# Optimization experiments

Hardware: AMD Instinct MI355X
Metric: run time of the kernel (lower is better)

Reference implementation:

```python
import jax, jax.numpy as jnp
import numpy as np

N = 50000      # nodes
E = 800000     # edges (avg degree 16)
F_IN = 512     # num_feature
H = 256        # nhid


def setup_inputs() -> dict:
    key = jax.random.key(0)
    ks = jax.random.split(key, 40)
    def p(k, shape):
        return jax.random.normal(k, shape, jnp.float32) * 0.05
    inp = {}
    inp["x"] = jax.random.normal(ks[0], (N, F_IN), jnp.float32)
    src = jax.random.randint(ks[1], (E,), 0, N, jnp.int32)
    dst = jax.random.randint(ks[2], (E,), 0, N, jnp.int32)
    inp["edge_index"] = jnp.stack([src, dst])  # [2, E]
    # GIN conv MLPs: Lin(din,H), ReLU, Lin(H,H). Weights stored [in, out].
    dims = [F_IN, H, H, H]
    i = 3
    for li, din in enumerate(dims, 1):
        inp[f"c{li}w1"] = p(ks[i], (din, H)); i += 1
        inp[f"c{li}b1"] = p(ks[i], (H,)); i += 1
        inp[f"c{li}w2"] = p(ks[i], (H, H)); i += 1
        inp[f"c{li}b2"] = p(ks[i], (H,)); i += 1
    # 2-layer LSTM, gate order i,f,g,o; single fused bias (b_ih + b_hh).
    for l in range(2):
        inp[f"lstm{l}_wih"] = p(ks[i], (H, 4 * H)); i += 1
        inp[f"lstm{l}_whh"] = p(ks[i], (H, 4 * H)); i += 1
        inp[f"lstm{l}_b"] = p(ks[i], (4 * H,)); i += 1
    inp["mlp_w"] = p(ks[i], (H, H)); i += 1
    inp["mlp_b"] = p(ks[i], (H,))
    return inp


def _gin(h, src, dst, w1, b1, w2, b2):
    # GINConv with eps=0: nn(x + sum_{j->i} x_j)
    agg = jax.ops.segment_sum(h[src], dst, num_segments=N)
    z = jax.nn.relu((h + agg) @ w1 + b1)
    return z @ w2 + b2


def _lstm_layer(seq, wih, whh, b):
    # seq: [T, N, H] -> hidden states [T, N, H]
    def step(carry, xt):
        h, c = carry
        g = xt @ wih + h @ whh + b
        i, f, gg, o = jnp.split(g, 4, axis=-1)
        c = jax.nn.sigmoid(f) * c + jax.nn.sigmoid(i) * jnp.tanh(gg)
        h = jax.nn.sigmoid(o) * jnp.tanh(c)
        return (h, c), h
    h0 = jnp.zeros((seq.shape[1], whh.shape[0]), seq.dtype)
    _, hs = jax.lax.scan(step, (h0, h0), seq)
    return hs


def reference(x, edge_index, c1w1, c1b1, c1w2, c1b2, c2w1, c2b1, c2w2, c2b2,
              c3w1, c3b1, c3w2, c3b2, c4w1, c4b1, c4w2, c4b2,
              lstm0_wih, lstm0_whh, lstm0_b, lstm1_wih, lstm1_whh, lstm1_b,
              mlp_w, mlp_b):
    src, dst = edge_index[0], edge_index[1]
    x1 = jax.nn.relu(_gin(x, src, dst, c1w1, c1b1, c1w2, c1b2))
    x2 = jax.nn.relu(_gin(x1, src, dst, c2w1, c2b1, c2w2, c2b2))
    x3 = jax.nn.relu(_gin(x2, src, dst, c3w1, c3b1, c3w2, c3b2))
    x4 = jax.nn.relu(_gin(x3, src, dst, c4w1, c4b1, c4w2, c4b2))
    # residual sums (in-place cascade as in the original)
    x2 = x2 + x1
    x3 = x3 + x2
    x4 = x4 + x3
    x_sum = x1 + x2 + x3 + x4
    stack = jnp.stack([x_sum, x1, x2, x3, x4])  # [5, N, H]
    x_avg = stack.mean(axis=0)
    x_max = stack.max(axis=0)
    seq = jnp.stack([x1, x2, x3, x4])  # [4, N, H]
    h = _lstm_layer(seq, lstm0_wih, lstm0_whh, lstm0_b)
    h = _lstm_layer(h, lstm1_wih, lstm1_whh, lstm1_b)
    x_lstm = h.mean(axis=0)
    # channel attention: relu(mlp(x_avg) + mlp(x_max) + mlp(x_lstm))
    return jax.nn.relu((x_avg + x_max + x_lstm) @ mlp_w + 3.0 * mlp_b)
```

## Files before the change

kernel.cpp:

```cpp
#include <hip/hip_runtime.h>

typedef unsigned int u32;
typedef unsigned short u16;

typedef __attribute__((ext_vector_type(8))) __bf16 bf16x8;
typedef __attribute__((ext_vector_type(4))) float f32x4;

__device__ __forceinline__ u16 f2bf(float f) {
  u32 u = __float_as_uint(f);
  u += 0x7fffu + ((u >> 16) & 1u);
  return (u16)(u >> 16);
}
__device__ __forceinline__ float bl(u32 u) { return __uint_as_float(u << 16); }
__device__ __forceinline__ float bh(u32 u) { return __uint_as_float(u & 0xffff0000u); }
__device__ __forceinline__ u32 pk2(float a, float b) { return (u32)f2bf(a) | ((u32)f2bf(b) << 16); }
__device__ __forceinline__ float fsig(float x) { return 1.f / (1.f + __expf(-x)); }
__device__ __forceinline__ float ftanh(float x) { return 1.f - 2.f / (__expf(2.f * x) + 1.f); }

#define GLDS16(gp, lp)                                                                  \
  __builtin_amdgcn_global_load_lds((const __attribute__((address_space(1))) u32*)(gp),  \
                                   (__attribute__((address_space(3))) u32*)(lp), 16, 0, 0)

struct WTargs {
  const float* src[13];
  u16* dst[13];
  int K[13];
  int Nc[13];
  int bstart[14];
};
__global__ __launch_bounds__(256) void k_wtall(WTargs wa) {
  int b = blockIdx.x;
  int w = 0;
  while (b >= wa.bstart[w + 1]) ++w;
  int i = (b - wa.bstart[w]) * 256 + threadIdx.x;
  int K = wa.K[w], Nc = wa.Nc[w];
  if (i >= K * Nc) return;
  int k = i / Nc, c = i - k * Nc;
  wa.dst[w][(size_t)c * K + k] = f2bf(wa.src[w][i]);
}

__global__ __launch_bounds__(256) void k_x2bf(const float* __restrict__ x, u16* __restrict__ xb, int total8) {
  int i = blockIdx.x * 256 + threadIdx.x;
  if (i >= total8) return;
  size_t o = (size_t)i * 8;
  float4 a = *(const float4*)(x + o), b = *(const float4*)(x + o + 4);
  uint4 v;
  v.x = pk2(a.x, a.y); v.y = pk2(a.z, a.w); v.z = pk2(b.x, b.y); v.w = pk2(b.z, b.w);
  *(uint4*)(xb + o) = v;
}

__global__ void k_hist(const int* __restrict__ dst, int* __restrict__ deg, int E) {
  int e = blockIdx.x * 256 + threadIdx.x;
  if (e < E) atomicAdd(&deg[dst[e]], 1);
}
__global__ __launch_bounds__(1024) void k_scan1(const int* __restrict__ deg, int* __restrict__ rs,
                                                int* __restrict__ bsum, int n) {
  __shared__ int buf[1024];
  int t = threadIdx.x, idx = blockIdx.x * 1024 + t;
  int v = idx < n ? deg[idx] : 0;
  buf[t] = v;
  __syncthreads();
  for (int off = 1; off < 1024; off <<= 1) {
    int u = t >= off ? buf[t - off] : 0;
    __syncthreads();
    buf[t] += u;
    __syncthreads();
  }
  if (idx < n) rs[idx + 1] = buf[t];
  if (t == 1023) bsum[blockIdx.x] = buf[1023];
}
__global__ void k_scan2(int* bsum, int nb) {
  if (threadIdx.x == 0) {
    int s = 0;
    for (int b = 0; b < nb; ++b) { s += bsum[b]; bsum[b] = s; }
  }
}
__global__ void k_scan3(const int* __restrict__ bsum, int* __restrict__ rs,
                        int* __restrict__ cursor, int n) {
  int i = blockIdx.x * 256 + threadIdx.x;
  if (i >= n) return;
  int b = i >> 10;
  int add = b ? bsum[b - 1] : 0;
  int v = rs[i + 1] + add;
  int d = cursor[i];
  rs[i + 1] = v;
  cursor[i] = v - d;
  if (i == 0) rs[0] = 0;
}
__global__ void k_scatter(const int* __restrict__ src, const int* __restrict__ dst,
                          int* __restrict__ cursor, int* __restrict__ esrc, int E) {
  int e = blockIdx.x * 256 + threadIdx.x;
  if (e < E) {
    int p = atomicAdd(&cursor[dst[e]], 1);
    esrc[p] = src[e];
  }
}

__global__ __launch_bounds__(256) void k_aggbr(const u16* __restrict__ y, const int* __restrict__ rowstart,
                                               const int* __restrict__ esrc, const float* __restrict__ b1,
                                               u16* __restrict__ z, int Nn, int base, int rows) {
  int lane = threadIdx.x & 63, wid = threadIdx.x >> 6;
  int r = blockIdx.x * 4 + wid;
  if (r >= rows) return;
  int node = base + r;
  const int cb = lane * 4;
  u16* orow = z + (size_t)r * 256 + cb;
  if (node >= Nn) { *(uint2*)orow = uint2{0, 0}; return; }
  float acc[4];
  {
    uint2 v = *(const uint2*)(y + (size_t)node * 256 + cb);
    acc[0] = bl(v.x); acc[1] = bh(v.x); acc[2] = bl(v.y); acc[3] = bh(v.y);
  }
  int s = rowstart[node], e = rowstart[node + 1];
  int j = s;
  for (; j + 3 < e; j += 4) {
    uint2 v0 = *(const uint2*)(y + (size_t)esrc[j] * 256 + cb);
    uint2 v1 = *(const uint2*)(y + (size_t)esrc[j + 1] * 256 + cb);
    uint2 v2 = *(const uint2*)(y + (size_t)esrc[j + 2] * 256 + cb);
    uint2 v3 = *(const uint2*)(y + (size_t)esrc[j + 3] * 256 + cb);
    acc[0] += (bl(v0.x) + bl(v1.x)) + (bl(v2.x) + bl(v3.x));
    acc[1] += (bh(v0.x) + bh(v1.x)) + (bh(v2.x) + bh(v3.x));
    acc[2] += (bl(v0.y) + bl(v1.y)) + (bl(v2.y) + bl(v3.y));
    acc[3] += (bh(v0.y) + bh(v1.y)) + (bh(v2.y) + bh(v3.y));
  }
  for (; j < e; ++j) {
    uint2 v = *(const uint2*)(y + (size_t)esrc[j] * 256 + cb);
    acc[0] += bl(v.x); acc[1] += bh(v.x); acc[2] += bl(v.y); acc[3] += bh(v.y);
  }
  float4 bb = *(const float4*)(b1 + cb);
  acc[0] = fmaxf(acc[0] + bb.x, 0.f);
  acc[1] = fmaxf(acc[1] + bb.y, 0.f);
  acc[2] = fmaxf(acc[2] + bb.z, 0.f);
  acc[3] = fmaxf(acc[3] + bb.w, 0.f);
  uint2 o;
  o.x = pk2(acc[0], acc[1]); o.y = pk2(acc[2], acc[3]);
  *(uint2*)orow = o;
}

__global__ __launch_bounds__(256) void k_agg256(const u16* __restrict__ h,
                                                const int* __restrict__ rowstart,
                                                const int* __restrict__ esrc,
                                                u16* __restrict__ out, int Nn, int base, int rows) {
  int lane = threadIdx.x & 63, wid = threadIdx.x >> 6;
  int r = blockIdx.x * 4 + wid;
  if (r >= rows) return;
  int node = base + r;
  const int cb = lane * 4;
  u16* orow = out + (size_t)r * 256 + cb;
  if (node >= Nn) { *(uint2*)orow = uint2{0, 0}; return; }
  float acc[4];
  {
    uint2 v = *(const uint2*)(h + (size_t)node * 256 + cb);
    acc[0] = bl(v.x); acc[1] = bh(v.x); acc[2] = bl(v.y); acc[3] = bh(v.y);
  }
  int s = rowstart[node], e = rowstart[node + 1];
  int j = s;
  for (; j + 3 < e; j += 4) {
    uint2 v0 = *(const uint2*)(h + (size_t)esrc[j] * 256 + cb);
    uint2 v1 = *(const uint2*)(h + (size_t)esrc[j + 1] * 256 + cb);
    uint2 v2 = *(const uint2*)(h + (size_t)esrc[j + 2] * 256 + cb);
    uint2 v3 = *(const uint2*)(h + (size_t)esrc[j + 3] * 256 + cb);
    acc[0] += (bl(v0.x) + bl(v1.x)) + (bl(v2.x) + bl(v3.x));
    acc[1] += (bh(v0.x) + bh(v1.x)) + (bh(v2.x) + bh(v3.x));
    acc[2] += (bl(v0.y) + bl(v1.y)) + (bl(v2.y) + bl(v3.y));
    acc[3] += (bh(v0.y) + bh(v1.y)) + (bh(v2.y) + bh(v3.y));
  }
  for (; j < e; ++j) {
    uint2 v = *(const uint2*)(h + (size_t)esrc[j] * 256 + cb);
    acc[0] += bl(v.x); acc[1] += bh(v.x); acc[2] += bl(v.y); acc[3] += bh(v.y);
  }
  uint2 o;
  o.x = pk2(acc[0], acc[1]); o.y = pk2(acc[2], acc[3]);
  *(uint2*)orow = o;
}

template <int BN, int MODE>
__global__ __launch_bounds__(256) void k_gemm(const u16* __restrict__ A1, const u16* __restrict__ B1, int K1,
                                              const u16* __restrict__ A2, const u16* __restrict__ B2, int K2,
                                              const float* __restrict__ bias, float bscale,
                                              void* __restrict__ outp, int Nout, int Mstore, int NT,
                                              u16* __restrict__ cstp, float* __restrict__ hsump,
                                              int first, int dosum) {
  constexpr int NF = BN / 32;
  __shared__ u16 Al[128 * 64];
  __shared__ u16 Bl[BN * 64];
  const int tid = threadIdx.x;
  const int lane = tid & 63, wid = tid >> 6;
  const int wr = wid >> 1, wc = wid & 1;
  const int nwg = gridDim.x;
  const int orig = blockIdx.x;
  const int q = nwg >> 3, rr8 = nwg & 7;
  const int xcd = orig & 7;
  const int wgid = (xcd < rr8 ? xcd * (q + 1) : rr8 * (q + 1) + (xcd - rr8) * q) + (orig >> 3);
  const int mtile = wgid / NT, ntile = wgid - mtile * NT;
  const int m0 = mtile * 128;
  const int n0 = ntile * BN;
  const int h0 = ntile * 32;
  const int l15 = lane & 15, l4 = lane >> 4;
  const int srow = lane >> 3;
  const int scol = ((lane & 7) ^ (lane >> 3)) * 8;
  const int rsw = l15 & 7;
  f32x4 acc[4][NF] = {};

  for (int s = 0; s < 2; ++s) {
    const u16* A = s ? A2 : A1;
    const u16* B = s ? B2 : B1;
    const int K = s ? K2 : K1;
    if (A == nullptr) continue;
    for (int k0 = 0; k0 < K; k0 += 64) {
      __syncthreads();
#pragma unroll
      for (int p = 0; p < 4; ++p) {
        int r = m0 + p * 32 + wid * 8 + srow;
        GLDS16(A + (size_t)r * K + k0 + scol, &Al[(p * 32 + wid * 8) * 64]);
      }
#pragma unroll
      for (int p = 0; p < NF; ++p) {
        int r;
        if constexpr (MODE == 3) r = p * 256 + h0 + wid * 8 + srow;
        else r = n0 + p * 32 + wid * 8 + srow;
        GLDS16(B + (size_t)r * K + k0 + scol, &Bl[(p * 32 + wid * 8) * 64]);
      }
      __syncthreads();
#pragma unroll
      for (int ks = 0; ks < 2; ++ks) {
        const int sp = (((ks * 4 + l4) ^ rsw)) * 8;
        bf16x8 af[4], bfr[NF];
#pragma unroll
        for (int m = 0; m < 4; ++m)
          af[m] = *(const bf16x8*)&Al[(wr * 64 + m * 16 + l15) * 64 + sp];
#pragma unroll
        for (int n = 0; n < NF; ++n) {
          int trow;
          if constexpr (MODE == 3) trow = n * 32 + wc * 16 + l15;
          else trow = wc * (BN / 2) + n * 16 + l15;
          bfr[n] = *(const bf16x8*)&Bl[trow * 64 + sp];
        }
#pragma unroll
        for (int m = 0; m < 4; ++m)
#pragma unroll
          for (int n = 0; n < NF; ++n)
            acc[m][n] = __builtin_amdgcn_mfma_f32_16x16x32_bf16(af[m], bfr[n], acc[m][n], 0, 0, 0);
      }
    }
  }

  if constexpr (MODE == 3) {
    const int hcol = h0 + wc * 16 + l15;
    const float bi = bias[hcol], bf2 = bias[256 + hcol];
    const float bg = bias[512 + hcol], bo = bias[768 + hcol];
    u16* hout = (u16*)outp;
#pragma unroll
    for (int m = 0; m < 4; ++m) {
      int gr0 = m0 + wr * 64 + m * 16 + l4 * 4;
#pragma unroll
      for (int r = 0; r < 4; ++r) {
        int gr = gr0 + r;
        if (gr >= Mstore) continue;
        float gi = acc[m][0][r] + bi;
        float gf = acc[m][1][r] + bf2;
        float gg = acc[m][2][r] + bg;
        float go = acc[m][3][r] + bo;
        size_t o = (size_t)gr * 256 + hcol;
        float nc = fsig(gi) * ftanh(gg);
        if (!first) nc += fsig(gf) * bl((u32)cstp[o]);
        cstp[o] = f2bf(nc);
        nc = bl((u32)f2bf(nc));
        float h = fsig(go) * ftanh(nc);
        hout[o] = f2bf(h);
        if (dosum) {
          if (first) hsump[o] = h;
          else hsump[o] += h;
        }
      }
    }
    return;
  }

#pragma unroll
  for (int m = 0; m < 4; ++m) {
    int gr0 = m0 + wr * 64 + m * 16 + l4 * 4;
#pragma unroll
    for (int n = 0; n < NF; ++n) {
      int gc = n0 + wc * (BN / 2) + n * 16 + l15;
      float bb = bias ? bias[gc] * bscale : 0.f;
#pragma unroll
      for (int r = 0; r < 4; ++r) {
        int gr = gr0 + r;
        if (gr >= Mstore) continue;
        float v = acc[m][n][r] + bb;
        if (MODE >= 1) v = fmaxf(v, 0.f);
        if (MODE == 2) ((float*)outp)[(size_t)gr * Nout + gc] = v;
        else ((u16*)outp)[(size_t)gr * Nout + gc] = f2bf(v);
      }
    }
  }
}

__global__ __launch_bounds__(256) void k_cascade(const u16* __restrict__ x1, u16* __restrict__ x2,
                                                 u16* __restrict__ x3, u16* __restrict__ x4, int total4) {
  int i = blockIdx.x * 256 + threadIdx.x;
  if (i >= total4) return;
  size_t o = (size_t)i * 4;
  uint2 v1 = *(const uint2*)(x1 + o), v2 = *(const uint2*)(x2 + o);
  uint2 v3 = *(const uint2*)(x3 + o), v4 = *(const uint2*)(x4 + o);
  float a1[4] = {bl(v1.x), bh(v1.x), bl(v1.y), bh(v1.y)};
  float a2[4] = {bl(v2.x), bh(v2.x), bl(v2.y), bh(v2.y)};
  float a3[4] = {bl(v3.x), bh(v3.x), bl(v3.y), bh(v3.y)};
  float a4[4] = {bl(v4.x), bh(v4.x), bl(v4.y), bh(v4.y)};
  float y2[4], y3[4], y4[4];
#pragma unroll
  for (int j = 0; j < 4; ++j) {
    y2[j] = a2[j] + a1[j];
    y3[j] = a3[j] + y2[j];
    y4[j] = a4[j] + y3[j];
  }
  *(uint2*)(x2 + o) = uint2{pk2(y2[0], y2[1]), pk2(y2[2], y2[3])};
  *(uint2*)(x3 + o) = uint2{pk2(y3[0], y3[1]), pk2(y3[2], y3[3])};
  *(uint2*)(x4 + o) = uint2{pk2(y4[0], y4[1]), pk2(y4[2], y4[3])};
}

__global__ __launch_bounds__(256) void k_sfin(const u16* __restrict__ x1, const u16* __restrict__ x2,
                                              const u16* __restrict__ x3, const u16* __restrict__ x4,
                                              const float* __restrict__ hsum, u16* __restrict__ sb,
                                              int total4) {
  int i = blockIdx.x * 256 + threadIdx.x;
  if (i >= total4) return;
  size_t o = (size_t)i * 4;
  uint2 v1 = *(const uint2*)(x1 + o), v2 = *(const uint2*)(x2 + o);
  uint2 v3 = *(const uint2*)(x3 + o), v4 = *(const uint2*)(x4 + o);
  float4 hh = *(const float4*)(hsum + o);
  float r0 = 1.4f * (bl(v1.x) + bl(v2.x) + bl(v3.x) + bl(v4.x)) + 0.25f * hh.x;
  float r1 = 1.4f * (bh(v1.x) + bh(v2.x) + bh(v3.x) + bh(v4.x)) + 0.25f * hh.y;
  float r2 = 1.4f * (bl(v1.y) + bl(v2.y) + bl(v3.y) + bl(v4.y)) + 0.25f * hh.z;
  float r3 = 1.4f * (bh(v1.y) + bh(v2.y) + bh(v3.y) + bh(v4.y)) + 0.25f * hh.w;
  *(uint2*)(sb + o) = uint2{pk2(r0, r1), pk2(r2, r3)};
}

extern "C" void kernel_launch(void* const* d_in, const int* in_sizes, int n_in,
                              void* d_out, int out_size, void* d_ws, size_t ws_size,
                              hipStream_t stream) {
  (void)n_in; (void)out_size;
  const int N = in_sizes[0] / 512;
  const int E = in_sizes[1] / 2;
  const int Mpad = ((N + 127) / 128) * 128;
  auto al128 = [](int v) { return ((v + 127) / 128) * 128; };

  const float* x = (const float*)d_in[0];
  const int* ei = (const int*)d_in[1];
  const int* esrc_in = ei;
  const int* edst_in = ei + E;

  size_t off = 0;
  auto alloc = [&](size_t bytes) { size_t o = off; off += (bytes + 255) & ~(size_t)255; return o; };
  char* ws = (char*)d_ws;
  const size_t szH = (size_t)Mpad * 256 * 2;
  const size_t szXB = (size_t)Mpad * 512 * 2;
  const int widx[13] = {2, 4, 6, 8, 10, 12, 14, 16, 18, 19, 21, 22, 24};
  const int wK[13] = {512, 256, 256, 256, 256, 256, 256, 256, 256, 256, 256, 256, 256};
  const int wN[13] = {256, 256, 256, 256, 256, 256, 256, 256, 1024, 1024, 1024, 1024, 256};
  size_t wt_o[13];
  for (int i = 0; i < 13; ++i) wt_o[i] = alloc((size_t)wK[i] * wN[i] * 2);
  size_t rowstart_o = alloc((size_t)(N + 1) * 4);
  size_t cursor_o = alloc((size_t)N * 4);
  size_t bsum_o = alloc(256 * 4);
  size_t esrc_o = alloc((size_t)E * 4);
  size_t x_o[4];
  for (int t = 0; t < 4; ++t) x_o[t] = alloc(szH);
  int McC = al128((Mpad + 3) / 4);
  int McL = al128((Mpad + 7) / 8);
  {
    const int ccand[3] = {Mpad, al128((Mpad + 1) / 2), al128((Mpad + 3) / 4)};
    const int lcand[4] = {al128((Mpad + 1) / 2), 16384, 8192, al128((Mpad + 7) / 8)};
    bool done = false;
    for (int ci = 0; ci < 3 && !done; ++ci) {
      for (int li = 0; li < 4 && !done; ++li) {
        size_t cneed = szXB + szH + (size_t)ccand[ci] * 512;
        size_t lneed = (size_t)lcand[li] * 5120;
        size_t tmp = cneed > lneed ? cneed : lneed;
        if (off + tmp + (1u << 20) <= ws_size) { McC = ccand[ci]; McL = lcand[li]; done = true; }
      }
    }
  }
  const size_t hb = (size_t)McL * 256 * 2;
  const size_t fb = (size_t)McL * 256 * 4;
  size_t lstm_sz = 8 * hb + fb;
  size_t conv_sz = szXB + szH + (size_t)McC * 512;
  size_t tmp_o = alloc(lstm_sz > conv_sz ? lstm_sz : conv_sz);
  if (off > ws_size) return;

  u16* wt[13];
  for (int i = 0; i < 13; ++i) wt[i] = (u16*)(ws + wt_o[i]);
  int* rowstart = (int*)(ws + rowstart_o);
  int* cursor = (int*)(ws + cursor_o);
  int* bsum = (int*)(ws + bsum_o);
  int* esrc = (int*)(ws + esrc_o);
  u16* xl[4];
  for (int t = 0; t < 4; ++t) xl[t] = (u16*)(ws + x_o[t]);
  u16* xb = (u16*)(ws + tmp_o);
  u16* y1 = (u16*)(ws + tmp_o + szXB);
  u16* zC = (u16*)(ws + tmp_o + szXB + szH);
  u16* h0s[4];
  for (int t = 0; t < 4; ++t) h0s[t] = (u16*)(ws + tmp_o + t * hb);
  u16* h1p[2] = {(u16*)(ws + tmp_o + 4 * hb), (u16*)(ws + tmp_o + 5 * hb)};
  u16* cst = (u16*)(ws + tmp_o + 6 * hb);
  u16* sbc = (u16*)(ws + tmp_o + 7 * hb);
  float* hsum = (float*)(ws + tmp_o + 8 * hb);

  WTargs wa;
  int bacc = 0;
  for (int i = 0; i < 13; ++i) {
    wa.src[i] = (const float*)d_in[widx[i]];
    wa.dst[i] = wt[i];
    wa.K[i] = wK[i];
    wa.Nc[i] = wN[i];
    wa.bstart[i] = bacc;
    bacc += (wK[i] * wN[i] + 255) / 256;
  }
  wa.bstart[13] = bacc;
  k_wtall<<<bacc, 256, 0, stream>>>(wa);
  k_x2bf<<<(N * 64 + 255) / 256, 256, 0, stream>>>(x, xb, N * 64);
  if (Mpad > N) hipMemsetAsync(xb + (size_t)N * 512, 0, (size_t)(Mpad - N) * 512 * 2, stream);
  hipMemsetAsync(cursor, 0, (size_t)N * 4, stream);
  k_hist<<<(E + 255) / 256, 256, 0, stream>>>(edst_in, cursor, E);
  const int nb = (N + 1023) / 1024;
  k_scan1<<<nb, 1024, 0, stream>>>(cursor, rowstart, bsum, N);
  k_scan2<<<1, 64, 0, stream>>>(bsum, nb);
  k_scan3<<<(N + 255) / 256, 256, 0, stream>>>(bsum, rowstart, cursor, N);
  k_scatter<<<(E + 255) / 256, 256, 0, stream>>>(esrc_in, edst_in, cursor, esrc, E);

  auto gemm = [&](const u16* A1, const u16* B1, int K1, const u16* A2, const u16* B2, int K2,
                  const float* bias, float bscale, void* out, int Nout, int rows, int Mstore,
                  int mode) {
    dim3 b(256);
    if (mode == 0) {
      int NT = Nout / 128;
      dim3 g((rows / 128) * NT);
      k_gemm<128, 0><<<g, b, 0, stream>>>(A1, B1, K1, A2, B2, K2, bias, bscale, out, Nout, Mstore,
                                          NT, nullptr, nullptr, 0, 0);
    } else if (mode == 1) {
      int NT = Nout / 128;
      dim3 g((rows / 128) * NT);
      k_gemm<128, 1><<<g, b, 0, stream>>>(A1, B1, K1, A2, B2, K2, bias, bscale, out, Nout, Mstore,
                                          NT, nullptr, nullptr, 0, 0);
    } else {
      int NT = Nout / 64;
      dim3 g((rows / 128) * NT);
      k_gemm<64, 2><<<g, b, 0, stream>>>(A1, B1, K1, A2, B2, K2, bias, bscale, out, Nout, Mstore,
                                         NT, nullptr, nullptr, 0, 0);
    }
  };
  auto lstm_step = [&](const u16* xt, const u16* wih, const u16* hprev, const u16* whh,
                       const float* bias, u16* hout, float* hsumP, int rows, int first, int dosum) {
    dim3 g((rows / 128) * 8), b(256);
    k_gemm<128, 3><<<g, b, 0, stream>>>(xt, wih, 256, hprev, whh, 256, bias, 1.f,
                                        hout, 256, rows, 8, cst, hsumP, first, dosum);
  };

  gemm(xb, wt[0], 512, nullptr, nullptr, 0, nullptr, 0.f, y1, 256, Mpad, Mpad, 0);
  for (int base = 0; base < Mpad; base += McC) {
    int rows = Mpad - base < McC ? Mpad - base : McC;
    int ab = (rows + 3) / 4;
    k_aggbr<<<ab, 256, 0, stream>>>(y1, rowstart, esrc, (const float*)d_in[3], zC, N, base, rows);
    gemm(zC, wt[1], 256, nullptr, nullptr, 0, (const float*)d_in[5], 1.f,
         xl[0] + (size_t)base * 256, 256, rows, rows, 1);
  }
  for (int l = 1; l < 4; ++l) {
    const int cb1[4] = {3, 7, 11, 15}, cb2[4] = {5, 9, 13, 17};
    for (int base = 0; base < Mpad; base += McC) {
      int rows = Mpad - base < McC ? Mpad - base : McC;
      int ab = (rows + 3) / 4;
      k_agg256<<<ab, 256, 0, stream>>>(xl[l - 1], rowstart, esrc, zC, N, base, rows);
      gemm((u16*)zC, wt[2 * l], 256, nullptr, nullptr, 0, (const float*)d_in[cb1[l]], 1.f,
           y1, 256, rows, rows, 1);
      gemm(y1, wt[2 * l + 1], 256, nullptr, nullptr, 0, (const float*)d_in[cb2[l]], 1.f,
           xl[l] + (size_t)base * 256, 256, rows, rows, 1);
    }
  }
  k_cascade<<<(Mpad * 64 + 255) / 256, 256, 0, stream>>>(xl[0], xl[1], xl[2], xl[3], Mpad * 64);

  const float* b_l0 = (const float*)d_in[20];
  const float* b_l1 = (const float*)d_in[23];
  const float* b_mlp = (const float*)d_in[25];
  for (int base = 0; base < Mpad; base += McL) {
    int rows = Mpad - base < McL ? Mpad - base : McL;
    const size_t boff = (size_t)base * 256;
    for (int t = 0; t < 4; ++t)
      lstm_step(xl[t] + boff, wt[8], t ? h0s[t - 1] : nullptr, wt[9], b_l0,
                h0s[t], nullptr, rows, t == 0, 0);
    for (int t = 0; t < 4; ++t)
      lstm_step(h0s[t], wt[10], t ? h1p[(t + 1) & 1] : nullptr, wt[11], b_l1,
                h1p[t & 1], hsum, rows, t == 0, 1);
    k_sfin<<<(rows * 64 + 255) / 256, 256, 0, stream>>>(xl[0] + boff, xl[1] + boff, xl[2] + boff,
                                                        xl[3] + boff, hsum, sbc, rows * 64);
    int st = N - base;
    if (st > rows) st = rows;
    if (st > 0)
      gemm(sbc, wt[12], 256, nullptr, nullptr, 0, b_mlp, 3.f,
           (float*)d_out + boff, 256, rows, st, 2);
  }
}
```

Baseline: 1.547 ms.

## Double-buffer GEMM LDS tiles to overlap global loads with MFMA

The GEMM kernel now keeps two LDS buffers for the A and B tiles. It prefetches the next K-tile with global_load_lds and waits only on the older loads through explicit vmcnt waits before computing the current tile. The two K segments are merged into one tile sequence so the prefetch carries across them. This aims to hide global memory latency behind the matrix math, at the cost of twice the LDS, which may lower occupancy. It also relies on hand-written waitcnt and barrier ordering being correct.

After: 1.824 ms. +17.9%, slower.

```diff
diff --git a/kernel.cpp b/kernel.cpp
--- a/kernel.cpp
+++ b/kernel.cpp
@@ -20,6 +20,13 @@
 #define GLDS16(gp, lp)                                                                  \
   __builtin_amdgcn_global_load_lds((const __attribute__((address_space(1))) u32*)(gp),  \
                                    (__attribute__((address_space(3))) u32*)(lp), 16, 0, 0)
+
+template <int N>
+__device__ __forceinline__ void waitvm() {
+  if constexpr (N == 8) asm volatile("s_waitcnt vmcnt(8)" ::: "memory");
+  else if constexpr (N == 6) asm volatile("s_waitcnt vmcnt(6)" ::: "memory");
+  else asm volatile("s_waitcnt vmcnt(0)" ::: "memory");
+}
 
 struct WTargs {
   const float* src[13];
@@ -182,8 +189,9 @@
                                               u16* __restrict__ cstp, float* __restrict__ hsump,
                                               int first, int dosum) {
   constexpr int NF = BN / 32;
-  __shared__ u16 Al[128 * 64];
-  __shared__ u16 Bl[BN * 64];
+  constexpr int LOADS = 4 + NF;
+  __shared__ u16 Al[2][128 * 64];
+  __shared__ u16 Bl[2][BN * 64];
   const int tid = threadIdx.x;
   const int lane = tid & 63, wid = tid >> 6;
   const int wr = wid >> 1, wc = wid & 1;
@@ -202,47 +210,61 @@
   const int rsw = l15 & 7;
   f32x4 acc[4][NF] = {};
 
-  for (int s = 0; s < 2; ++s) {
-    const u16* A = s ? A2 : A1;
-    const u16* B = s ? B2 : B1;
-    const int K = s ? K2 : K1;
-    if (A == nullptr) continue;
-    for (int k0 = 0; k0 < K; k0 += 64) {
-      __syncthreads();
-#pragma unroll
-      for (int p = 0; p < 4; ++p) {
-        int r = m0 + p * 32 + wid * 8 + srow;
-        GLDS16(A + (size_t)r * K + k0 + scol, &Al[(p * 32 + wid * 8) * 64]);
+  const int nt1 = K1 / 64;
+  const int nt2 = A2 ? K2 / 64 : 0;
+  const int nt = nt1 + nt2;
+
+  auto stage = [&](int buf, int t) {
+    const u16* A; const u16* B; int K; int k0;
+    if (t < nt1) { A = A1; B = B1; K = K1; k0 = t * 64; }
+    else { A = A2; B = B2; K = K2; k0 = (t - nt1) * 64; }
+#pragma unroll
+    for (int p = 0; p < 4; ++p) {
+      int r = m0 + p * 32 + wid * 8 + srow;
+      GLDS16(A + (size_t)r * K + k0 + scol, &Al[buf][(p * 32 + wid * 8) * 64]);
+    }
+#pragma unroll
+    for (int p = 0; p < NF; ++p) {
+      int r;
+      if constexpr (MODE == 3) r = p * 256 + h0 + wid * 8 + srow;
+      else r = n0 + p * 32 + wid * 8 + srow;
+      GLDS16(B + (size_t)r * K + k0 + scol, &Bl[buf][(p * 32 + wid * 8) * 64]);
+    }
+  };
+
+  stage(0, 0);
+  int cur = 0;
+  for (int t = 0; t < nt; ++t) {
+    if (t + 1 < nt) {
+      stage(cur ^ 1, t + 1);
+      waitvm<LOADS>();
+    } else {
+      waitvm<0>();
+    }
+    __builtin_amdgcn_s_barrier();
+#pragma unroll
+    for (int ks = 0; ks < 2; ++ks) {
+      const int sp = (((ks * 4 + l4) ^ rsw)) * 8;
+      bf16x8 af[4], bfr[NF];
+#pragma unroll
+      for (int m = 0; m < 4; ++m)
+        af[m] = *(const bf16x8*)&Al[cur][(wr * 64 + m * 16 + l15) * 64 + sp];
+#pragma unroll
+      for (int n = 0; n < NF; ++n) {
+        int trow;
+        if constexpr (MODE == 3) trow = n * 32 + wc * 16 + l15;
+        else trow = wc * (BN / 2) + n * 16 + l15;
+        bfr[n] = *(const bf16x8*)&Bl[cur][trow * 64 + sp];
       }
 #pragma unroll
-      for (int p = 0; p < NF; ++p) {
-        int r;
-        if constexpr (MODE == 3) r = p * 256 + h0 + wid * 8 + srow;
-        else r = n0 + p * 32 + wid * 8 + srow;
-        GLDS16(B + (size_t)r * K + k0 + scol, &Bl[(p * 32 + wid * 8) * 64]);
-      }
-      __syncthreads();
-#pragma unroll
-      for (int ks = 0; ks < 2; ++ks) {
-        const int sp = (((ks * 4 + l4) ^ rsw)) * 8;
-        bf16x8 af[4], bfr[NF];
-#pragma unroll
-        for (int m = 0; m < 4; ++m)
-          af[m] = *(const bf16x8*)&Al[(wr * 64 + m * 16 + l15) * 64 + sp];
-#pragma unroll
-        for (int n = 0; n < NF; ++n) {
-          int trow;
-          if constexpr (MODE == 3) trow = n * 32 + wc * 16 + l15;
-          else trow = wc * (BN / 2) + n * 16 + l15;
-          bfr[n] = *(const bf16x8*)&Bl[trow * 64 + sp];
-        }
-#pragma unroll
-        for (int m = 0; m < 4; ++m)
-#pragma unroll
-          for (int n = 0; n < NF; ++n)
-            acc[m][n] = __builtin_amdgcn_mfma_f32_16x16x32_bf16(af[m], bfr[n], acc[m][n], 0, 0, 0);
-      }
-    }
+      for (int m = 0; m < 4; ++m)
+#pragma unroll
+        for (int n = 0; n < NF; ++n)
+          acc[m][n] = __builtin_amdgcn_mfma_f32_16x16x32_bf16(af[m], bfr[n], acc[m][n], 0, 0, 0);
+    }
+    asm volatile("" ::: "memory");
+    __builtin_amdgcn_s_barrier();
+    cur ^= 1;
   }
 
   if constexpr (MODE == 3) {
```
